# Kernel tuning notes

Measured on AMD Instinct MI355X. Metric: run time of the kernel, lower is better.

## Reference

```python
import jax, jax.numpy as jnp
from jax import lax
import numpy as np

B, CIN, L = 16, 512, 1024
COUT, K = 1024, 5          # conv out channels (GLU halves to 512), kernel size
DW = 512                    # word_feat == attn_channels == img_conv channels
HW = 196                    # 14*14 image feature locations


def setup_inputs() -> dict:
    key = jax.random.key(0)
    ks = jax.random.split(key, 8)
    s = 0.02
    return {
        "x": jax.random.normal(ks[0], (B, CIN, L), jnp.float32),
        "word_embed": jax.random.normal(ks[1], (B, L, DW), jnp.float32),
        "img_conv": jax.random.normal(ks[2], (B, DW, 14, 14), jnp.float32),
        "prev_attn": jnp.zeros((B, L, HW), jnp.float32),  # passed through, unused
        "conv_v": jax.random.normal(ks[3], (COUT, CIN, K), jnp.float32) * s,
        "conv_g": jnp.ones((COUT,), jnp.float32),
        "conv_b": jnp.zeros((COUT,), jnp.float32),
        "fc1_w": jax.random.normal(ks[4], (DW, DW), jnp.float32) * s,
        "fc1_b": jnp.zeros((DW,), jnp.float32),
        "fc2_w": jax.random.normal(ks[5], (DW, DW), jnp.float32) * s,
        "fc2_b": jnp.zeros((DW,), jnp.float32),
    }


def reference(x, word_embed, img_conv, prev_attn,
              conv_v, conv_g, conv_b, fc1_w, fc1_b, fc2_w, fc2_b):
    k = conv_v.shape[-1]
    # weight norm (PyTorch default dim=0): w = g * v / ||v||_{(in,k)}
    v_norm = jnp.sqrt(jnp.sum(conv_v * conv_v, axis=(1, 2), keepdims=True))
    w = (conv_g[:, None, None] / v_norm) * conv_v
    # Conv1d, padding=k-1 on both sides -> length L + k - 1 after ConvS2S trim
    y = lax.conv_general_dilated(x, w, window_strides=(1,),
                                 padding=[(k - 1, k - 1)],
                                 dimension_numbers=("NCH", "OIH", "NCH"))
    y = y + conv_b[None, :, None]
    # dropout is identity in eval mode
    a, b = jnp.split(y, 2, axis=1)          # GLU over channel dim
    h = a * jax.nn.sigmoid(b)
    h = h[:, :, : -(k - 1)]                  # [B, DW, L]
    identity_attn = h
    # attn_fc1 on [B, L, DW] then add word embeddings
    q = jnp.einsum("bcl,ac->bla", h, fc1_w) + fc1_b + word_embed  # [B, L, DW]
    feat = img_conv.reshape(img_conv.shape[0], img_conv.shape[1], -1)  # [B, DW, HW]
    score = jnp.einsum("bla,bap->blp", q, feat)   # [B, L, HW]
    attn = jax.nn.softmax(score, axis=-1)         # softmax over image locations
    ctx = jnp.einsum("blp,bap->bla", attn, feat)  # [B, L, DW]
    o = jnp.einsum("bla,ca->blc", ctx, fc2_w) + fc2_b
    out = o.transpose(0, 2, 1) + identity_attn
    # identity.shape == out.shape (input_feat == output_feat/2) -> no downsample
    out = out + x
    return (out, word_embed, img_conv, attn)
```

## Files before the change

### kernel.cpp

```cpp
#include <hip/hip_runtime.h>
#include <math.h>

#define NB   16
#define NCIN 512
#define NL   1024
#define NCOUT 1024
#define NK   5
#define NDW  512
#define NHW  196
#define NP   208
#define NPK  224
#define NLG  1028

typedef unsigned short ushort_t;
typedef unsigned int uint_t;
typedef __attribute__((ext_vector_type(8))) short bf16x8;
typedef __attribute__((ext_vector_type(4))) float f32x4;

static __device__ __forceinline__ ushort_t f2bf(float f) {
  uint_t u = __builtin_bit_cast(uint_t, f);
  u += 0x7fff + ((u >> 16) & 1);
  return (ushort_t)(u >> 16);
}
static __device__ __forceinline__ float bf2f(ushort_t u) {
  uint_t v = ((uint_t)u) << 16;
  return __builtin_bit_cast(float, v);
}

#define BARM()     asm volatile("s_barrier" ::: "memory")
#define WAITVM8()  asm volatile("s_waitcnt vmcnt(8)" ::: "memory")
#define WAITVM0()  asm volatile("s_waitcnt vmcnt(0)" ::: "memory")
#define WAITLGKM0() asm volatile("s_waitcnt lgkmcnt(0)" ::: "memory")

static __device__ __forceinline__ void gld16(const ushort_t* g, ushort_t* l) {
  __builtin_amdgcn_global_load_lds(
      (const __attribute__((address_space(1))) unsigned int*)g,
      (__attribute__((address_space(3))) unsigned int*)l, 16, 0, 0);
}

__global__ __launch_bounds__(256) void wnorm_kernel(
    const float* __restrict__ v, const float* __restrict__ g,
    ushort_t* __restrict__ wperm) {
  const int o = blockIdx.x;
  const float* vr = v + (size_t)o * (NCIN * NK);
  float s = 0.f;
  for (int j = threadIdx.x; j < NCIN * NK; j += 256) {
    float t = vr[j];
    s += t * t;
  }
  for (int off = 32; off; off >>= 1) s += __shfl_down(s, off, 64);
  __shared__ float red[4];
  __shared__ float scale_s;
  const int wid = threadIdx.x >> 6;
  if ((threadIdx.x & 63) == 0) red[wid] = s;
  __syncthreads();
  if (threadIdx.x == 0) {
    float tot = red[0] + red[1] + red[2] + red[3];
    scale_s = g[o] / sqrtf(tot);
  }
  __syncthreads();
  const float scale = scale_s;
  const int isB = (o >= NDW) ? 1 : 0;
  const int c = o - isB * NDW;
  const int j = (c >> 5) * 64 + isB * 32 + (c & 31);
#pragma unroll
  for (int dk = 0; dk < NK; ++dk) {
    for (int ci = threadIdx.x; ci < NCIN; ci += 256) {
      wperm[((size_t)dk * NCOUT + j) * NCIN + ci] = f2bf(vr[ci * NK + dk] * scale);
    }
  }
}

__global__ __launch_bounds__(256) void xpose_kernel(
    const float* __restrict__ x, ushort_t* __restrict__ xT) {
  const int b = blockIdx.z;
  const int ci0 = blockIdx.y * 64;
  const int l0 = blockIdx.x * 64;
  const int tid = threadIdx.x;
  __shared__ float t[64][65];
  const float* xb = x + ((size_t)b * NCIN + ci0) * NL + l0;
#pragma unroll
  for (int r = 0; r < 4; ++r) {
    int row = r * 16 + (tid >> 4);
    int col = (tid & 15) * 4;
    float4 v = *(const float4*)&xb[(size_t)row * NL + col];
    t[row][col + 0] = v.x; t[row][col + 1] = v.y;
    t[row][col + 2] = v.z; t[row][col + 3] = v.w;
  }
  __syncthreads();
  ushort_t* xo = xT + ((size_t)b * NLG + l0 + 4) * NCIN + ci0;
#pragma unroll
  for (int r = 0; r < 4; ++r) {
    int lrow = r * 16 + (tid >> 4);
    int cic = (tid & 15) * 4;
    ushort4 o4;
    o4.x = f2bf(t[cic + 0][lrow]);
    o4.y = f2bf(t[cic + 1][lrow]);
    o4.z = f2bf(t[cic + 2][lrow]);
    o4.w = f2bf(t[cic + 3][lrow]);
    *(ushort4*)&xo[(size_t)lrow * NCIN + cic] = o4;
  }
  if (blockIdx.x == 0) {
    for (int i = tid; i < 4 * 64; i += 256) {
      int rr = i >> 6, cc = i & 63;
      xT[((size_t)b * NLG + rr) * NCIN + ci0 + cc] = 0;
    }
  }
}

__global__ __launch_bounds__(256) void wcvt_kernel(
    const float* __restrict__ w1, const float* __restrict__ w2,
    ushort_t* __restrict__ w1bf, ushort_t* __restrict__ w2bf) {
  const int i = (blockIdx.x * 256 + threadIdx.x) * 4;
  {
    float4 v = *(const float4*)&w1[i];
    ushort4 o; o.x = f2bf(v.x); o.y = f2bf(v.y); o.z = f2bf(v.z); o.w = f2bf(v.w);
    *(ushort4*)&w1bf[i] = o;
  }
  {
    float4 v = *(const float4*)&w2[i];
    ushort4 o; o.x = f2bf(v.x); o.y = f2bf(v.y); o.z = f2bf(v.z); o.w = f2bf(v.w);
    *(ushort4*)&w2bf[i] = o;
  }
}

__global__ __launch_bounds__(256) void ftrans_kernel(
    const float* __restrict__ feat, ushort_t* __restrict__ fThi,
    ushort_t* __restrict__ fTlo, ushort_t* __restrict__ fbf) {
  const int b = blockIdx.y;
  const int a0 = blockIdx.x * 64;
  const int tid = threadIdx.x;
  __shared__ float t[64][200];

  const float* fb_ = feat + ((size_t)b * NDW + a0) * NHW;
#pragma unroll
  for (int pp = 0; pp < 16; ++pp) {
    int row = pp * 4 + (tid >> 6);
#pragma unroll
    for (int cc = 0; cc < 4; ++cc) {
      int col = cc * 64 + (tid & 63);
      if (col < NHW) t[row][col] = fb_[(size_t)row * NHW + col];
    }
  }
  __syncthreads();

  for (int pp = 0; pp < 13; ++pp) {
    int p = pp * 16 + (tid >> 4);
    int j = (tid & 15) * 4;
    ushort4 hi4, lo4;
#pragma unroll
    for (int k = 0; k < 4; ++k) {
      float v = (p < NHW) ? t[j + k][p] : 0.f;
      ushort_t h = f2bf(v);
      float lof = v - bf2f(h);
      ushort_t l = f2bf(lof);
      ((ushort_t*)&hi4)[k] = h;
      ((ushort_t*)&lo4)[k] = l;
    }
    size_t base = ((size_t)b * NP + p) * NDW + a0 + j;
    *(ushort4*)&fThi[base] = hi4;
    *(ushort4*)&fTlo[base] = lo4;
  }

#pragma unroll
  for (int cc = 0; cc < 4; ++cc) {
    int col = cc * 64 + (tid & 63);
    if (col < NPK) {
#pragma unroll
      for (int rr = 0; rr < 16; ++rr) {
        int al = rr * 4 + (tid >> 6);
        float v = (col < NHW) ? t[al][col] : 0.f;
        fbf[((size_t)b * NDW + a0 + al) * NPK + col] = f2bf(v);
      }
    }
  }
}

__global__ __launch_bounds__(512, 2) void conv_glu_mfma(
    const ushort_t* __restrict__ xT, const ushort_t* __restrict__ wperm,
    const float* __restrict__ conv_b, ushort_t* __restrict__ hbfT) {
  const int bb = blockIdx.x >> 2;
  const int l0 = (blockIdx.x & 3) * 256;
  const int by = blockIdx.y;
  const int tid = threadIdx.x;
  const int wid = tid >> 6;
  const int lane = tid & 63;
  const int wm = wid >> 2;
  const int wn = wid & 3;
  const int quad = lane >> 4;
  const int l16 = lane & 15;
  const int sw = (l16 & 7) << 3;
  const int csrc = ((lane & 7) ^ (lane >> 3)) << 3;

  __shared__ ushort_t sA[2][256][64];
  __shared__ ushort_t sB[2][256][64];

  f32x4 acc[8][4];
#pragma unroll
  for (int mt = 0; mt < 8; ++mt)
#pragma unroll
    for (int nt = 0; nt < 4; ++nt) acc[mt][nt] = (f32x4){0.f, 0.f, 0.f, 0.f};

  const ushort_t* gAbase = xT + (size_t)(bb * NLG + l0) * NCIN;
  const int r0 = wid * 8 + (lane >> 3);
  ushort_t* lA0 = &sA[0][0][0] + (wid * 64 + lane) * 8;
  ushort_t* lB0 = &sB[0][0][0] + (wid * 64 + lane) * 8;

  auto stage = [&](int tt, int s) {
    const int dk = tt >> 3;
    const int ci0 = (tt & 7) << 6;
    const ushort_t* gA = gAbase + (size_t)dk * NCIN + ci0 + csrc;
    const ushort_t* gB = wperm + ((size_t)dk * NCOUT + by * 256) * NCIN + ci0 + csrc;
    ushort_t* lA = lA0 + s * (256 * 64);
    ushort_t* lB = lB0 + s * (256 * 64);
#pragma unroll
    for (int c = 0; c < 4; ++c) {
      gld16(gA + (size_t)(r0 + c * 64) * NCIN, lA + c * 4096);
      gld16(gB + (size_t)(r0 + c * 64) * NCIN, lB + c * 4096);
    }
  };

  stage(0, 0);
  stage(1, 1);
  WAITVM8();
  BARM();

  for (int t = 0; t < 40; ++t) {
    const int s = t & 1;
    bf16x8 af[4][2], bfr[4][2];

#pragma unroll
    for (int mt = 0; mt < 4; ++mt)
#pragma unroll
      for (int ks = 0; ks < 2; ++ks)
        af[mt][ks] = *(const bf16x8*)&sA[s][wm * 128 + mt * 16 + l16]
                                        [(ks * 32 + quad * 8) ^ sw];
#pragma unroll
    for (int nt = 0; nt < 2; ++nt)
#pragma unroll
      for (int ks = 0; ks < 2; ++ks)
        bfr[nt][ks] = *(const bf16x8*)&sB[s][wn * 64 + nt * 16 + l16]
                                         [(ks * 32 + quad * 8) ^ sw];
    BARM();
    __builtin_amdgcn_s_setprio(1);
#pragma unroll
    for (int ks = 0; ks < 2; ++ks)
#pragma unroll
      for (int nt = 0; nt < 2; ++nt)
#pragma unroll
        for (int mt = 0; mt < 4; ++mt)
          acc[mt][nt] = __builtin_amdgcn_mfma_f32_16x16x32_bf16(
              af[mt][ks], bfr[nt][ks], acc[mt][nt], 0, 0, 0);
    __builtin_amdgcn_s_setprio(0);
    BARM();

#pragma unroll
    for (int nt = 2; nt < 4; ++nt)
#pragma unroll
      for (int ks = 0; ks < 2; ++ks)
        bfr[nt][ks] = *(const bf16x8*)&sB[s][wn * 64 + nt * 16 + l16]
                                         [(ks * 32 + quad * 8) ^ sw];
    BARM();
    __builtin_amdgcn_s_setprio(1);
#pragma unroll
    for (int ks = 0; ks < 2; ++ks)
#pragma unroll
      for (int nt = 2; nt < 4; ++nt)
#pragma unroll
        for (int mt = 0; mt < 4; ++mt)
          acc[mt][nt] = __builtin_amdgcn_mfma_f32_16x16x32_bf16(
              af[mt][ks], bfr[nt][ks], acc[mt][nt], 0, 0, 0);
    __builtin_amdgcn_s_setprio(0);
    BARM();

#pragma unroll
    for (int mt = 0; mt < 4; ++mt)
#pragma unroll
      for (int ks = 0; ks < 2; ++ks)
        af[mt][ks] = *(const bf16x8*)&sA[s][wm * 128 + (4 + mt) * 16 + l16]
                                        [(ks * 32 + quad * 8) ^ sw];
    BARM();
    __builtin_amdgcn_s_setprio(1);
#pragma unroll
    for (int ks = 0; ks < 2; ++ks)
#pragma unroll
      for (int nt = 0; nt < 2; ++nt)
#pragma unroll
        for (int mt = 0; mt < 4; ++mt)
          acc[4 + mt][nt] = __builtin_amdgcn_mfma_f32_16x16x32_bf16(
              af[mt][ks], bfr[nt][ks], acc[4 + mt][nt], 0, 0, 0);
    __builtin_amdgcn_s_setprio(0);
    WAITLGKM0();
    BARM();

    if (t < 38) stage(t + 2, s);
    __builtin_amdgcn_s_setprio(1);
#pragma unroll
    for (int ks = 0; ks < 2; ++ks)
#pragma unroll
      for (int nt = 2; nt < 4; ++nt)
#pragma unroll
        for (int mt = 0; mt < 4; ++mt)
          acc[4 + mt][nt] = __builtin_amdgcn_mfma_f32_16x16x32_bf16(
              af[mt][ks], bfr[nt][ks], acc[4 + mt][nt], 0, 0, 0);
    __builtin_amdgcn_s_setprio(0);

    if (t < 39) {
      if (t < 38) { WAITVM8(); } else { WAITVM0(); }
      BARM();
    }
  }

#pragma unroll
  for (int nt = 0; nt < 2; ++nt) {
    const int c = by * 128 + wn * 32 + nt * 16 + l16;
    const float ba = conv_b[c];
    const float bg = conv_b[c + NDW];
#pragma unroll
    for (int mt = 0; mt < 8; ++mt) {
      const int lg = l0 + wm * 128 + mt * 16 + quad * 4;
      ushort_t* ho = hbfT + ((size_t)bb * NL + lg) * NDW + c;
#pragma unroll
      for (int r = 0; r < 4; ++r) {
        float aa = acc[mt][nt][r] + ba;
        float gg = acc[mt][nt + 2][r] + bg;
        float hv = aa * (1.f / (1.f + __expf(-gg)));
        ho[(size_t)r * NDW] = f2bf(hv);
      }
    }
  }
}

__global__ __launch_bounds__(256, 2) void attn_fused(
    const ushort_t* __restrict__ hbfT, const ushort_t* __restrict__ w1bf,
    const float* __restrict__ fb1, const float* __restrict__ we,
    const ushort_t* __restrict__ fThi, const ushort_t* __restrict__ fTlo,
    const ushort_t* __restrict__ fbf, float* __restrict__ out_attn,
    ushort_t* __restrict__ ctx_bf) {
  const int b  = blockIdx.y;
  const int l0 = blockIdx.x * 64;
  const int tid = threadIdx.x;
  const int wid = tid >> 6;
  const int lane = tid & 63;
  const int quad = lane >> 4;
  const int l16 = lane & 15;

  __shared__ ushort_t smem[36224];
  ushort_t* wS = smem;
  ushort_t* fh = smem + 16640;
  ushort_t* fl = smem + 24128;
  ushort_t* qh = smem + 31616;
  ushort_t* ql = smem + 33920;
  ushort_t* pa = smem;
  ushort_t* fb = smem + 14848;

  uint4 hreg[16];
  {
    const ushort_t* hrow =
        hbfT + ((size_t)b * NL + l0 + wid * 16 + l16) * NDW + quad * 8;
#pragma unroll
    for (int cs = 0; cs < 16; ++cs)
      hreg[cs] = *(const uint4*)(hrow + cs * 32);
  }

  f32x4 acc[13];
#pragma unroll
  for (int nt = 0; nt < 13; ++nt) acc[nt] = (f32x4){0.f, 0.f, 0.f, 0.f};

  for (int kc = 0; kc < 16; ++kc) {
    const int a0 = kc * 32;

    float wev[2][4];
    float bias[2];
#pragma unroll
    for (int nt = 0; nt < 2; ++nt) {
      const int a = a0 + nt * 16 + l16;
      bias[nt] = fb1[a];
#pragma unroll
      for (int r = 0; r < 4; ++r) {
        const int l = l0 + wid * 16 + quad * 4 + r;
        wev[nt][r] = we[((size_t)b * NL + l) * NDW + a];
      }
    }

    __syncthreads();
    {
      int r = tid >> 2, seg = tid & 3;
#pragma unroll
      for (int it = 0; it < 4; ++it) {
        int row = it * 64 + r;
        if (row < NP) {
          size_t fsrc = ((size_t)b * NP + row) * NDW + a0 + seg * 8;
          *(uint4*)&fh[row * 36 + seg * 8] = *(const uint4*)(fThi + fsrc);
          *(uint4*)&fl[row * 36 + seg * 8] = *(const uint4*)(fTlo + fsrc);
        }
      }
#pragma unroll
      for (int it = 0; it < 8; ++it) {
        int lin = tid + it * 256;
        int rr = lin >> 6, ss = lin & 63;
        *(uint4*)&wS[rr * 520 + ss * 8] =
            *(const uint4*)(w1bf + (size_t)(a0 + rr) * NDW + ss * 8);
      }
    }
    __syncthreads();

    f32x4 aq[2][2];
    aq[0][0] = aq[0][1] = aq[1][0] = aq[1][1] = (f32x4){0.f, 0.f, 0.f, 0.f};
#pragma unroll
    for (int cs = 0; cs < 16; ++cs) {
      bf16x8 af = __builtin_bit_cast(bf16x8, hreg[cs]);
#pragma unroll
      for (int nt = 0; nt < 2; ++nt) {
        bf16x8 bw = *(const bf16x8*)&wS[(nt * 16 + l16) * 520 + cs * 32 + quad * 8];
        aq[cs & 1][nt] = __builtin_amdgcn_mfma_f32_16x16x32_bf16(af, bw, aq[cs & 1][nt], 0, 0, 0);
      }
    }
#pragma unroll
    for (int nt = 0; nt < 2; ++nt) {
#pragma unroll
      for (int r = 0; r < 4; ++r) {
        float qv = aq[0][nt][r] + aq[1][nt][r] + bias[nt] + wev[nt][r];
        ushort_t h = f2bf(qv);
        const int row = wid * 16 + quad * 4 + r;
        qh[row * 36 + nt * 16 + l16] = h;
        ql[row * 36 + nt * 16 + l16] = f2bf(qv - bf2f(h));
      }
    }
    __syncthreads();

    bf16x8 ah = *(const bf16x8*)&qh[(wid * 16 + l16) * 36 + quad * 8];
    bf16x8 al = *(const bf16x8*)&ql[(wid * 16 + l16) * 36 + quad * 8];
#pragma unroll
    for (int nt = 0; nt < 13; ++nt) {
      bf16x8 bh = *(const bf16x8*)&fh[(nt * 16 + l16) * 36 + quad * 8];
      bf16x8 bl = *(const bf16x8*)&fl[(nt * 16 + l16) * 36 + quad * 8];
      acc[nt] = __builtin_amdgcn_mfma_f32_16x16x32_bf16(ah, bh, acc[nt], 0, 0, 0);
      acc[nt] = __builtin_amdgcn_mfma_f32_16x16x32_bf16(al, bh, acc[nt], 0, 0, 0);
      acc[nt] = __builtin_amdgcn_mfma_f32_16x16x32_bf16(ah, bl, acc[nt], 0, 0, 0);
    }
  }

  const bool v12 = (l16 < 4);
#pragma unroll
  for (int r = 0; r < 4; ++r) {
    float mx = -1e30f;
#pragma unroll
    for (int nt = 0; nt < 12; ++nt) mx = fmaxf(mx, acc[nt][r]);
    if (v12) mx = fmaxf(mx, acc[12][r]);
#pragma unroll
    for (int off = 1; off < 16; off <<= 1) mx = fmaxf(mx, __shfl_xor(mx, off, 16));
    float ex[13];
    float sum = 0.f;
#pragma unroll
    for (int nt = 0; nt < 12; ++nt) { ex[nt] = __expf(acc[nt][r] - mx); sum += ex[nt]; }
    ex[12] = v12 ? __expf(acc[12][r] - mx) : 0.f;
    sum += ex[12];
#pragma unroll
    for (int off = 1; off < 16; off <<= 1) sum += __shfl_xor(sum, off, 16);
    const float inv = 1.f / sum;
    const int l = l0 + wid * 16 + quad * 4 + r;
    float* ao = out_attn + ((size_t)b * NL + l) * NHW;
#pragma unroll
    for (int nt = 0; nt < 13; ++nt) {
      float av = ex[nt] * inv;
      acc[nt][r] = av;
      int p = nt * 16 + l16;
      if (p < NHW) ao[p] = av;
    }
  }

  __syncthreads();

#pragma unroll
  for (int r = 0; r < 4; ++r) {
    const int row = wid * 16 + quad * 4 + r;
#pragma unroll
    for (int nt = 0; nt < 13; ++nt) {
      int p = nt * 16 + l16;
      pa[row * 232 + p] = (p < NHW) ? f2bf(acc[nt][r]) : (ushort_t)0;
    }
    pa[row * 232 + 208 + l16] = 0;
  }

  for (int ac = 0; ac < 8; ++ac) {
    const int a0 = ac * 64;
    __syncthreads();
#pragma unroll
    for (int it = 0; it < 7; ++it) {
      int lin = tid + it * 256;
      int rr = lin / 28, ss = lin % 28;
      *(uint4*)&fb[rr * 232 + ss * 8] =
          *(const uint4*)(fbf + ((size_t)b * NDW + a0 + rr) * NPK + ss * 8);
    }
    __syncthreads();
    f32x4 ca[4];
#pragma unroll
    for (int nt = 0; nt < 4; ++nt) ca[nt] = (f32x4){0.f, 0.f, 0.f, 0.f};
#pragma unroll
    for (int ks = 0; ks < 7; ++ks) {
      bf16x8 af = *(const bf16x8*)&pa[(wid * 16 + l16) * 232 + ks * 32 + quad * 8];
#pragma unroll
      for (int nt = 0; nt < 4; ++nt) {
        bf16x8 bv = *(const bf16x8*)&fb[(nt * 16 + l16) * 232 + ks * 32 + quad * 8];
        ca[nt] = __builtin_amdgcn_mfma_f32_16x16x32_bf16(af, bv, ca[nt], 0, 0, 0);
      }
    }
#pragma unroll
    for (int nt = 0; nt < 4; ++nt) {
      const int a = a0 + nt * 16 + l16;
#pragma unroll
      for (int r = 0; r < 4; ++r) {
        const int l = l0 + wid * 16 + quad * 4 + r;
        ctx_bf[((size_t)b * NL + l) * NDW + a] = f2bf(ca[nt][r]);
      }
    }
  }
}

__global__ __launch_bounds__(256, 2) void fc2_mfma(
    const ushort_t* __restrict__ w2bf, const ushort_t* __restrict__ ctx_bf,
    const float* __restrict__ fb2, const ushort_t* __restrict__ hbfT,
    const float* __restrict__ x, float* __restrict__ out0) {
  const int b  = blockIdx.z;
  const int c0 = blockIdx.y * 128;
  const int l0 = blockIdx.x * 128;
  const int tid = threadIdx.x;
  const int wid = tid >> 6;
  const int lane = tid & 63;
  const int wl = wid & 1;
  const int wc = wid >> 1;
  const int quad = lane >> 4;
  const int l16 = lane & 15;

  __shared__ ushort_t la[128][72];
  __shared__ ushort_t lb[128][72];

  f32x4 acc[4][4];
#pragma unroll
  for (int mt = 0; mt < 4; ++mt)
#pragma unroll
    for (int nt = 0; nt < 4; ++nt) acc[mt][nt] = (f32x4){0.f, 0.f, 0.f, 0.f};

  for (int a0 = 0; a0 < NDW; a0 += 64) {
    __syncthreads();
#pragma unroll
    for (int it = 0; it < 4; ++it) {
      int t = tid + it * 256;
      int r = t >> 3, seg = t & 7;
      *(uint4*)&la[r][seg * 8] = *(const uint4*)(w2bf + (size_t)(c0 + r) * NDW + a0 + seg * 8);
    }
#pragma unroll
    for (int it = 0; it < 4; ++it) {
      int t = tid + it * 256;
      int r = t >> 3, seg = t & 7;
      *(uint4*)&lb[r][seg * 8] =
          *(const uint4*)(ctx_bf + ((size_t)b * NL + l0 + r) * NDW + a0 + seg * 8);
    }
    __syncthreads();
#pragma unroll
    for (int ks = 0; ks < 2; ++ks) {
      bf16x8 af[4];
#pragma unroll
      for (int mt = 0; mt < 4; ++mt)
        af[mt] = *(const bf16x8*)&la[wl * 64 + mt * 16 + l16][ks * 32 + quad * 8];
#pragma unroll
      for (int nt = 0; nt < 4; ++nt) {
        bf16x8 bf = *(const bf16x8*)&lb[wc * 64 + nt * 16 + l16][ks * 32 + quad * 8];
#pragma unroll
        for (int mt = 0; mt < 4; ++mt)
          acc[mt][nt] = __builtin_amdgcn_mfma_f32_16x16x32_bf16(af[mt], bf, acc[mt][nt], 0, 0, 0);
      }
    }
  }

#pragma unroll
  for (int mt = 0; mt < 4; ++mt) {
    const int cb = c0 + wl * 64 + mt * 16 + quad * 4;
    float4 bias4 = *(const float4*)&fb2[cb];
#pragma unroll
    for (int nt = 0; nt < 4; ++nt) {
      const int l = l0 + wc * 64 + nt * 16 + l16;
      ushort4 h4 = *(const ushort4*)&hbfT[((size_t)b * NL + l) * NDW + cb];
      const float bias[4] = {bias4.x, bias4.y, bias4.z, bias4.w};
      const ushort_t hs[4] = {h4.x, h4.y, h4.z, h4.w};
#pragma unroll
      for (int r = 0; r < 4; ++r) {
        size_t idx = ((size_t)b * NDW + cb + r) * NL + l;
        out0[idx] = acc[mt][nt][r] + bias[r] + bf2f(hs[r]) + x[idx];
      }
    }
  }
}

extern "C" void kernel_launch(void* const* d_in, const int* in_sizes, int n_in,
                              void* d_out, int out_size, void* d_ws, size_t ws_size,
                              hipStream_t stream) {
  const float* x      = (const float*)d_in[0];
  const float* we     = (const float*)d_in[1];
  const float* img    = (const float*)d_in[2];
  const float* conv_v = (const float*)d_in[4];
  const float* conv_g = (const float*)d_in[5];
  const float* conv_b = (const float*)d_in[6];
  const float* fc1_w  = (const float*)d_in[7];
  const float* fc1_b  = (const float*)d_in[8];
  const float* fc2_w  = (const float*)d_in[9];
  const float* fc2_b  = (const float*)d_in[10];

  float* out0     = (float*)d_out;
  float* out_we   = out0 + 8388608;
  float* out_img  = out_we + 8388608;
  float* out_attn = out_img + 1605632;

  ushort_t* wsu = (ushort_t*)d_ws;
  ushort_t* wperm = wsu;
  ushort_t* xT    = wsu + 2621440;
  ushort_t* ctx_b = wsu;
  ushort_t* hbfT  = wsu + 16777216;
  ushort_t* w1bf  = wsu + 25165824;
  ushort_t* w2bf  = wsu + 25165824 + 262144;
  ushort_t* fThi  = wsu + 25690112;
  ushort_t* fTlo  = wsu + 27394048;
  ushort_t* fbf   = wsu + 29097984;

  wnorm_kernel<<<dim3(NCOUT), 256, 0, stream>>>(conv_v, conv_g, wperm);
  xpose_kernel<<<dim3(16, 8, NB), 256, 0, stream>>>(x, xT);
  wcvt_kernel<<<dim3(256), 256, 0, stream>>>(fc1_w, fc2_w, w1bf, w2bf);
  ftrans_kernel<<<dim3(8, NB), 256, 0, stream>>>(img, fThi, fTlo, fbf);

  conv_glu_mfma<<<dim3(64, 4), 512, 0, stream>>>(xT, wperm, conv_b, hbfT);
  attn_fused<<<dim3(16, NB), 256, 0, stream>>>(hbfT, w1bf, fc1_b, we,
                                               fThi, fTlo, fbf, out_attn, ctx_b);
  fc2_mfma<<<dim3(8, 4, NB), 256, 0, stream>>>(w2bf, ctx_b, fc2_b, hbfT, x, out0);

  hipMemcpyAsync(out_we, we, (size_t)8388608 * sizeof(float),
                 hipMemcpyDeviceToDevice, stream);
  hipMemcpyAsync(out_img, img, (size_t)1605632 * sizeof(float),
                 hipMemcpyDeviceToDevice, stream);
}
```

Baseline: 435.5 us.

## Double-buffer attn_fused shared-memory stages with register prefetch

Restructures both loops in attn_fused to prefetch the next chunk's feature, fc1 weight, bias and word-embedding data into registers while the current chunk is computed. The prefetched data is then written to a second LDS buffer, which removes one barrier per iteration and hides global-load latency. The context loop is split into 32-wide chunks so the double buffer fits. In exchange, LDS use roughly doubles to about 135KB and launch bounds drop to one block per CU, cutting occupancy and adding register pressure.

```diff
diff --git a/kernel.cpp b/kernel.cpp
--- a/kernel.cpp
+++ b/kernel.cpp
@@ -331,7 +331,7 @@
   }
 }
 
-__global__ __launch_bounds__(256, 2) void attn_fused(
+__global__ __launch_bounds__(256, 1) void attn_fused(
     const ushort_t* __restrict__ hbfT, const ushort_t* __restrict__ w1bf,
     const float* __restrict__ fb1, const float* __restrict__ we,
     const ushort_t* __restrict__ fThi, const ushort_t* __restrict__ fTlo,
@@ -345,14 +345,66 @@
   const int quad = lane >> 4;
   const int l16 = lane & 15;
 
-  __shared__ ushort_t smem[36224];
-  ushort_t* wS = smem;
-  ushort_t* fh = smem + 16640;
-  ushort_t* fl = smem + 24128;
-  ushort_t* qh = smem + 31616;
-  ushort_t* ql = smem + 33920;
+  __shared__ ushort_t smem[67840];
+  ushort_t* qh = smem + 63232;
+  ushort_t* ql = smem + 65536;
   ushort_t* pa = smem;
-  ushort_t* fb = smem + 14848;
+
+  uint4 sfh[4], sfl[4], sw1[8];
+  float nwev[2][4], cwev[2][4];
+  float nbias[2], cbias[2];
+
+  auto load_stage = [&](int kc) {
+    const int a0 = kc * 32;
+#pragma unroll
+    for (int it = 0; it < 4; ++it) {
+      int row = it * 64 + (tid >> 2);
+      if (row < NP) {
+        size_t fsrc = ((size_t)b * NP + row) * NDW + a0 + (tid & 3) * 8;
+        sfh[it] = *(const uint4*)(fThi + fsrc);
+        sfl[it] = *(const uint4*)(fTlo + fsrc);
+      }
+    }
+#pragma unroll
+    for (int it = 0; it < 8; ++it) {
+      int lin = tid + it * 256;
+      sw1[it] = *(const uint4*)(w1bf + (size_t)(a0 + (lin >> 6)) * NDW + (lin & 63) * 8);
+    }
+#pragma unroll
+    for (int nt = 0; nt < 2; ++nt) {
+      const int a = a0 + nt * 16 + l16;
+      nbias[nt] = fb1[a];
+#pragma unroll
+      for (int r = 0; r < 4; ++r) {
+        const int l = l0 + wid * 16 + quad * 4 + r;
+        nwev[nt][r] = we[((size_t)b * NL + l) * NDW + a];
+      }
+    }
+  };
+  auto store_stage = [&](int s) {
+    ushort_t* fhs = smem + 33280 + s * 7488;
+    ushort_t* fls = smem + 48256 + s * 7488;
+    ushort_t* wSs = smem + s * 16640;
+#pragma unroll
+    for (int it = 0; it < 4; ++it) {
+      int row = it * 64 + (tid >> 2);
+      if (row < NP) {
+        *(uint4*)&fhs[row * 36 + (tid & 3) * 8] = sfh[it];
+        *(uint4*)&fls[row * 36 + (tid & 3) * 8] = sfl[it];
+      }
+    }
+#pragma unroll
+    for (int it = 0; it < 8; ++it) {
+      int lin = tid + it * 256;
+      *(uint4*)&wSs[(lin >> 6) * 520 + (lin & 63) * 8] = sw1[it];
+    }
+#pragma unroll
+    for (int nt = 0; nt < 2; ++nt) {
+      cbias[nt] = nbias[nt];
+#pragma unroll
+      for (int r = 0; r < 4; ++r) cwev[nt][r] = nwev[nt][r];
+    }
+  };
 
   uint4 hreg[16];
   {
@@ -363,47 +415,21 @@
       hreg[cs] = *(const uint4*)(hrow + cs * 32);
   }
 
+  load_stage(0);
+  store_stage(0);
+  __syncthreads();
+
   f32x4 acc[13];
 #pragma unroll
   for (int nt = 0; nt < 13; ++nt) acc[nt] = (f32x4){0.f, 0.f, 0.f, 0.f};
 
   for (int kc = 0; kc < 16; ++kc) {
-    const int a0 = kc * 32;
-
-    float wev[2][4];
-    float bias[2];
-#pragma unroll
-    for (int nt = 0; nt < 2; ++nt) {
-      const int a = a0 + nt * 16 + l16;
-      bias[nt] = fb1[a];
-#pragma unroll
-      for (int r = 0; r < 4; ++r) {
-        const int l = l0 + wid * 16 + quad * 4 + r;
-        wev[nt][r] = we[((size_t)b * NL + l) * NDW + a];
-      }
-    }
-
-    __syncthreads();
-    {
-      int r = tid >> 2, seg = tid & 3;
-#pragma unroll
-      for (int it = 0; it < 4; ++it) {
-        int row = it * 64 + r;
-        if (row < NP) {
-          size_t fsrc = ((size_t)b * NP + row) * NDW + a0 + seg * 8;
-          *(uint4*)&fh[row * 36 + seg * 8] = *(const uint4*)(fThi + fsrc);
-          *(uint4*)&fl[row * 36 + seg * 8] = *(const uint4*)(fTlo + fsrc);
-        }
-      }
-#pragma unroll
-      for (int it = 0; it < 8; ++it) {
-        int lin = tid + it * 256;
-        int rr = lin >> 6, ss = lin & 63;
-        *(uint4*)&wS[rr * 520 + ss * 8] =
-            *(const uint4*)(w1bf + (size_t)(a0 + rr) * NDW + ss * 8);
-      }
-    }
-    __syncthreads();
+    const int cur = kc & 1;
+    ushort_t* wSc = smem + cur * 16640;
+    ushort_t* fhc = smem + 33280 + cur * 7488;
+    ushort_t* flc = smem + 48256 + cur * 7488;
+
+    if (kc < 15) load_stage(kc + 1);
 
     f32x4 aq[2][2];
     aq[0][0] = aq[0][1] = aq[1][0] = aq[1][1] = (f32x4){0.f, 0.f, 0.f, 0.f};
@@ -412,7 +438,7 @@
       bf16x8 af = __builtin_bit_cast(bf16x8, hreg[cs]);
 #pragma unroll
       for (int nt = 0; nt < 2; ++nt) {
-        bf16x8 bw = *(const bf16x8*)&wS[(nt * 16 + l16) * 520 + cs * 32 + quad * 8];
+        bf16x8 bw = *(const bf16x8*)&wSc[(nt * 16 + l16) * 520 + cs * 32 + quad * 8];
         aq[cs & 1][nt] = __builtin_amdgcn_mfma_f32_16x16x32_bf16(af, bw, aq[cs & 1][nt], 0, 0, 0);
       }
     }
@@ -420,7 +446,7 @@
     for (int nt = 0; nt < 2; ++nt) {
 #pragma unroll
       for (int r = 0; r < 4; ++r) {
-        float qv = aq[0][nt][r] + aq[1][nt][r] + bias[nt] + wev[nt][r];
+        float qv = aq[0][nt][r] + aq[1][nt][r] + cbias[nt] + cwev[nt][r];
         ushort_t h = f2bf(qv);
         const int row = wid * 16 + quad * 4 + r;
         qh[row * 36 + nt * 16 + l16] = h;
@@ -433,12 +459,15 @@
     bf16x8 al = *(const bf16x8*)&ql[(wid * 16 + l16) * 36 + quad * 8];
 #pragma unroll
     for (int nt = 0; nt < 13; ++nt) {
-      bf16x8 bh = *(const bf16x8*)&fh[(nt * 16 + l16) * 36 + quad * 8];
-      bf16x8 bl = *(const bf16x8*)&fl[(nt * 16 + l16) * 36 + quad * 8];
+      bf16x8 bh = *(const bf16x8*)&fhc[(nt * 16 + l16) * 36 + quad * 8];
+      bf16x8 bl = *(const bf16x8*)&flc[(nt * 16 + l16) * 36 + quad * 8];
       acc[nt] = __builtin_amdgcn_mfma_f32_16x16x32_bf16(ah, bh, acc[nt], 0, 0, 0);
       acc[nt] = __builtin_amdgcn_mfma_f32_16x16x32_bf16(al, bh, acc[nt], 0, 0, 0);
       acc[nt] = __builtin_amdgcn_mfma_f32_16x16x32_bf16(ah, bl, acc[nt], 0, 0, 0);
     }
+
+    if (kc < 15) store_stage(cur ^ 1);
+    __syncthreads();
   }
 
   const bool v12 = (l16 < 4);
@@ -472,6 +501,26 @@
 
   __syncthreads();
 
+  uint4 sfb[4];
+  auto load_fb = [&](int ac) {
+#pragma unroll
+    for (int it = 0; it < 4; ++it) {
+      int lin = tid + it * 256;
+      if (lin < 896)
+        sfb[it] = *(const uint4*)(fbf +
+            ((size_t)b * NDW + ac * 32 + lin / 28) * NPK + (lin % 28) * 8);
+    }
+  };
+  auto store_fb = [&](int s) {
+    ushort_t* fbs = smem + 14848 + s * 7424;
+#pragma unroll
+    for (int it = 0; it < 4; ++it) {
+      int lin = tid + it * 256;
+      if (lin < 896)
+        *(uint4*)&fbs[(lin / 28) * 232 + (lin % 28) * 8] = sfb[it];
+    }
+  };
+
 #pragma unroll
   for (int r = 0; r < 4; ++r) {
     const int row = wid * 16 + quad * 4 + r;
@@ -482,39 +531,37 @@
     }
     pa[row * 232 + 208 + l16] = 0;
   }
-
-  for (int ac = 0; ac < 8; ++ac) {
-    const int a0 = ac * 64;
-    __syncthreads();
-#pragma unroll
-    for (int it = 0; it < 7; ++it) {
-      int lin = tid + it * 256;
-      int rr = lin / 28, ss = lin % 28;
-      *(uint4*)&fb[rr * 232 + ss * 8] =
-          *(const uint4*)(fbf + ((size_t)b * NDW + a0 + rr) * NPK + ss * 8);
-    }
-    __syncthreads();
-    f32x4 ca[4];
-#pragma unroll
-    for (int nt = 0; nt < 4; ++nt) ca[nt] = (f32x4){0.f, 0.f, 0.f, 0.f};
+  load_fb(0);
+  store_fb(0);
+  __syncthreads();
+
+  for (int ac = 0; ac < 16; ++ac) {
+    const int cur = ac & 1;
+    ushort_t* fbc = smem + 14848 + cur * 7424;
+    if (ac < 15) load_fb(ac + 1);
+
+    f32x4 ca[2];
+    ca[0] = ca[1] = (f32x4){0.f, 0.f, 0.f, 0.f};
 #pragma unroll
     for (int ks = 0; ks < 7; ++ks) {
       bf16x8 af = *(const bf16x8*)&pa[(wid * 16 + l16) * 232 + ks * 32 + quad * 8];
 #pragma unroll
-      for (int nt = 0; nt < 4; ++nt) {
-        bf16x8 bv = *(const bf16x8*)&fb[(nt * 16 + l16) * 232 + ks * 32 + quad * 8];
+      for (int nt = 0; nt < 2; ++nt) {
+        bf16x8 bv = *(const bf16x8*)&fbc[(nt * 16 + l16) * 232 + ks * 32 + quad * 8];
         ca[nt] = __builtin_amdgcn_mfma_f32_16x16x32_bf16(af, bv, ca[nt], 0, 0, 0);
       }
     }
 #pragma unroll
-    for (int nt = 0; nt < 4; ++nt) {
-      const int a = a0 + nt * 16 + l16;
+    for (int nt = 0; nt < 2; ++nt) {
+      const int a = ac * 32 + nt * 16 + l16;
 #pragma unroll
       for (int r = 0; r < 4; ++r) {
         const int l = l0 + wid * 16 + quad * 4 + r;
         ctx_bf[((size_t)b * NL + l) * NDW + a] = f2bf(ca[nt][r]);
       }
     }
+    if (ac < 15) store_fb(cur ^ 1);
+    __syncthreads();
   }
 }
 
```

After: 548.2 us. +25.9%, slower.

## Double-buffer attn_fused LDS staging with async global_load_lds and XOR swizzle

Applied to the files above, without the earlier changes.

Restructures both phases of the fused attention kernel so the next chunk's fc1 weights, image features and ctx features are prefetched into a second LDS buffer with direct global-to-LDS loads while the current chunk's MFMAs run. Padded layouts are replaced by XOR-swizzled unpadded layouts to avoid bank conflicts. The context phase is split into smaller 32-column chunks to fit double buffering. In exchange, LDS grows to about 128KB per block, which may reduce occupancy below two blocks per CU. The hand-placed waitcnt/barrier sequence also replaces the __syncthreads around the q tile, which risks a race on qh/ql.

```diff
diff --git a/kernel.cpp b/kernel.cpp
--- a/kernel.cpp
+++ b/kernel.cpp
@@ -27,9 +27,9 @@
   return __builtin_bit_cast(float, v);
 }
 
-#define BARM()     asm volatile("s_barrier" ::: "memory")
-#define WAITVM8()  asm volatile("s_waitcnt vmcnt(8)" ::: "memory")
-#define WAITVM0()  asm volatile("s_waitcnt vmcnt(0)" ::: "memory")
+#define BARM()      asm volatile("s_barrier" ::: "memory")
+#define WAITVM8()   asm volatile("s_waitcnt vmcnt(8)" ::: "memory")
+#define WAITVM0()   asm volatile("s_waitcnt vmcnt(0)" ::: "memory")
 #define WAITLGKM0() asm volatile("s_waitcnt lgkmcnt(0)" ::: "memory")
 
 static __device__ __forceinline__ void gld16(const ushort_t* g, ushort_t* l) {
@@ -344,15 +344,38 @@
   const int lane = tid & 63;
   const int quad = lane >> 4;
   const int l16 = lane & 15;
-
-  __shared__ ushort_t smem[36224];
-  ushort_t* wS = smem;
-  ushort_t* fh = smem + 16640;
-  ushort_t* fl = smem + 24128;
-  ushort_t* qh = smem + 31616;
-  ushort_t* ql = smem + 33920;
+  const int s_f = ((l16 & 3) + (l16 >> 2)) & 3;
+  const int wmask = (l16 & 7) << 3;
+
+  __shared__ ushort_t smem[64000];
+  ushort_t* qh = smem + 59392;
+  ushort_t* ql = smem + 61696;
   ushort_t* pa = smem;
-  ushort_t* fb = smem + 14848;
+
+  auto stage1 = [&](int kc, int s) {
+    const int a0 = kc * 32;
+    ushort_t* wSb = smem + s * 16384;
+    ushort_t* fhb = smem + 32768 + s * 6656;
+    ushort_t* flb = smem + 46080 + s * 6656;
+#pragma unroll
+    for (int rr = 0; rr < 8; ++rr) {
+      const int r = rr * 4 + wid;
+      gld16(w1bf + (size_t)(a0 + r) * NDW + ((lane * 8) ^ ((r & 7) << 3)),
+            wSb + r * 512 + lane * 8);
+    }
+#pragma unroll
+    for (int ii = 0; ii < 4; ++ii) {
+      const int i = ii * 4 + wid;
+      if (i < 13) {
+        const int row = i * 16 + (lane >> 2);
+        const int s4 = (row + (row >> 2)) & 3;
+        const size_t gsrc =
+            ((size_t)b * NP + row) * NDW + a0 + (((lane & 3) * 8) ^ (s4 << 3));
+        gld16(fThi + gsrc, fhb + i * 512 + lane * 8);
+        gld16(fTlo + gsrc, flb + i * 512 + lane * 8);
+      }
+    }
+  };
 
   uint4 hreg[16];
   {
@@ -363,15 +386,21 @@
       hreg[cs] = *(const uint4*)(hrow + cs * 32);
   }
 
+  stage1(0, 0);
+  __syncthreads();
+
   f32x4 acc[13];
 #pragma unroll
   for (int nt = 0; nt < 13; ++nt) acc[nt] = (f32x4){0.f, 0.f, 0.f, 0.f};
 
   for (int kc = 0; kc < 16; ++kc) {
+    const int cur = kc & 1;
+    const ushort_t* wSc = smem + cur * 16384;
+    const ushort_t* fhc = smem + 32768 + cur * 6656;
+    const ushort_t* flc = smem + 46080 + cur * 6656;
     const int a0 = kc * 32;
 
-    float wev[2][4];
-    float bias[2];
+    float wev[2][4], bias[2];
 #pragma unroll
     for (int nt = 0; nt < 2; ++nt) {
       const int a = a0 + nt * 16 + l16;
@@ -383,27 +412,7 @@
       }
     }
 
-    __syncthreads();
-    {
-      int r = tid >> 2, seg = tid & 3;
-#pragma unroll
-      for (int it = 0; it < 4; ++it) {
-        int row = it * 64 + r;
-        if (row < NP) {
-          size_t fsrc = ((size_t)b * NP + row) * NDW + a0 + seg * 8;
-          *(uint4*)&fh[row * 36 + seg * 8] = *(const uint4*)(fThi + fsrc);
-          *(uint4*)&fl[row * 36 + seg * 8] = *(const uint4*)(fTlo + fsrc);
-        }
-      }
-#pragma unroll
-      for (int it = 0; it < 8; ++it) {
-        int lin = tid + it * 256;
-        int rr = lin >> 6, ss = lin & 63;
-        *(uint4*)&wS[rr * 520 + ss * 8] =
-            *(const uint4*)(w1bf + (size_t)(a0 + rr) * NDW + ss * 8);
-      }
-    }
-    __syncthreads();
+    if (kc < 15) stage1(kc + 1, cur ^ 1);
 
     f32x4 aq[2][2];
     aq[0][0] = aq[0][1] = aq[1][0] = aq[1][1] = (f32x4){0.f, 0.f, 0.f, 0.f};
@@ -412,7 +421,8 @@
       bf16x8 af = __builtin_bit_cast(bf16x8, hreg[cs]);
 #pragma unroll
       for (int nt = 0; nt < 2; ++nt) {
-        bf16x8 bw = *(const bf16x8*)&wS[(nt * 16 + l16) * 520 + cs * 32 + quad * 8];
+        bf16x8 bw = *(const bf16x8*)&wSc[(nt * 16 + l16) * 512 +
+                                         ((cs * 32 + quad * 8) ^ wmask)];
         aq[cs & 1][nt] = __builtin_amdgcn_mfma_f32_16x16x32_bf16(af, bw, aq[cs & 1][nt], 0, 0, 0);
       }
     }
@@ -427,17 +437,25 @@
         ql[row * 36 + nt * 16 + l16] = f2bf(qv - bf2f(h));
       }
     }
-    __syncthreads();
+    WAITLGKM0();
+    __builtin_amdgcn_sched_barrier(0);
 
     bf16x8 ah = *(const bf16x8*)&qh[(wid * 16 + l16) * 36 + quad * 8];
     bf16x8 al = *(const bf16x8*)&ql[(wid * 16 + l16) * 36 + quad * 8];
+    const int fcol = (quad * 8) ^ (s_f << 3);
 #pragma unroll
     for (int nt = 0; nt < 13; ++nt) {
-      bf16x8 bh = *(const bf16x8*)&fh[(nt * 16 + l16) * 36 + quad * 8];
-      bf16x8 bl = *(const bf16x8*)&fl[(nt * 16 + l16) * 36 + quad * 8];
+      bf16x8 bh = *(const bf16x8*)&fhc[(nt * 16 + l16) * 32 + fcol];
+      bf16x8 bl = *(const bf16x8*)&flc[(nt * 16 + l16) * 32 + fcol];
       acc[nt] = __builtin_amdgcn_mfma_f32_16x16x32_bf16(ah, bh, acc[nt], 0, 0, 0);
       acc[nt] = __builtin_amdgcn_mfma_f32_16x16x32_bf16(al, bh, acc[nt], 0, 0, 0);
       acc[nt] = __builtin_amdgcn_mfma_f32_16x16x32_bf16(ah, bl, acc[nt], 0, 0, 0);
+    }
+
+    if (kc < 15) {
+      WAITLGKM0();
+      WAITVM0();
+      BARM();
     }
   }
 
@@ -472,6 +490,25 @@
 
   __syncthreads();
 
+  auto stage2 = [&](int ac, int s) {
+    const int a0c = ac * 32;
+    ushort_t* fbb = smem + 14848 + s * 7168;
+#pragma unroll
+    for (int ii = 0; ii < 4; ++ii) {
+      const int i = ii * 4 + wid;
+      if (i < 14) {
+        const int byte0 = i * 1024 + lane * 16;
+        const unsigned q64 = (unsigned)byte0 >> 6;
+        const int row = (int)(q64 / 7u);
+        const int colb = (int)(q64 - (unsigned)row * 7u) * 64 + (byte0 & 63);
+        const int cu = colb >> 1;
+        const int s4 = (row + (row >> 2)) & 3;
+        gld16(fbf + ((size_t)b * NDW + a0c + row) * NPK + (cu ^ (s4 << 3)),
+              fbb + i * 512 + lane * 8);
+      }
+    }
+  };
+
 #pragma unroll
   for (int r = 0; r < 4; ++r) {
     const int row = wid * 16 + quad * 4 + r;
@@ -482,38 +519,39 @@
     }
     pa[row * 232 + 208 + l16] = 0;
   }
-
-  for (int ac = 0; ac < 8; ++ac) {
-    const int a0 = ac * 64;
-    __syncthreads();
-#pragma unroll
-    for (int it = 0; it < 7; ++it) {
-      int lin = tid + it * 256;
-      int rr = lin / 28, ss = lin % 28;
-      *(uint4*)&fb[rr * 232 + ss * 8] =
-          *(const uint4*)(fbf + ((size_t)b * NDW + a0 + rr) * NPK + ss * 8);
-    }
-    __syncthreads();
-    f32x4 ca[4];
-#pragma unroll
-    for (int nt = 0; nt < 4; ++nt) ca[nt] = (f32x4){0.f, 0.f, 0.f, 0.f};
+  stage2(0, 0);
+  __syncthreads();
+
+  for (int ac = 0; ac < 16; ++ac) {
+    const int cur = ac & 1;
+    const ushort_t* fbc = smem + 14848 + cur * 7168;
+    if (ac < 15) stage2(ac + 1, cur ^ 1);
+
+    f32x4 ca[2];
+    ca[0] = ca[1] = (f32x4){0.f, 0.f, 0.f, 0.f};
 #pragma unroll
     for (int ks = 0; ks < 7; ++ks) {
       bf16x8 af = *(const bf16x8*)&pa[(wid * 16 + l16) * 232 + ks * 32 + quad * 8];
 #pragma unroll
-      for (int nt = 0; nt < 4; ++nt) {
-        bf16x8 bv = *(const bf16x8*)&fb[(nt * 16 + l16) * 232 + ks * 32 + quad * 8];
+      for (int nt = 0; nt < 2; ++nt) {
+        bf16x8 bv = *(const bf16x8*)&fbc[(nt * 16 + l16) * 224 +
+                                         ((ks * 32 + quad * 8) ^ (s_f << 3))];
         ca[nt] = __builtin_amdgcn_mfma_f32_16x16x32_bf16(af, bv, ca[nt], 0, 0, 0);
       }
     }
 #pragma unroll
-    for (int nt = 0; nt < 4; ++nt) {
-      const int a = a0 + nt * 16 + l16;
+    for (int nt = 0; nt < 2; ++nt) {
+      const int a = ac * 32 + nt * 16 + l16;
 #pragma unroll
       for (int r = 0; r < 4; ++r) {
         const int l = l0 + wid * 16 + quad * 4 + r;
         ctx_bf[((size_t)b * NL + l) * NDW + a] = f2bf(ca[nt][r]);
       }
+    }
+    if (ac < 15) {
+      WAITLGKM0();
+      WAITVM0();
+      BARM();
     }
   }
 }
```

New measurement: 391.6 us. 10.1% less time.
